# Kernel tuning notes

Measured on AMD Instinct MI355X. Metric: run time of the kernel, lower is better.

## Reference

```python
import jax, jax.numpy as jnp
import numpy as np

B, IN_DIM, CTRL, N_LOC, LOC_SZ, OUT = 2048, 512, 512, 65536, 64, 1
EPS = 1e-8


def setup_inputs() -> dict:
    key = jax.random.key(0)
    ks = jax.random.split(key, 11)
    s = 0.02
    return {
        "x": jax.random.normal(ks[0], (B, IN_DIM), dtype=jnp.float32),
        # Controller: h = tanh(x W_h + b_h), gate = x W_g + b_g
        "W_h": jax.random.normal(ks[1], (IN_DIM, CTRL), dtype=jnp.float32) * s,
        "b_h": jnp.zeros((CTRL,), dtype=jnp.float32),
        "W_g": jax.random.normal(ks[2], (IN_DIM, 1), dtype=jnp.float32) * s,
        "b_g": jnp.zeros((1,), dtype=jnp.float32),
        # Head read-key net: key = tanh(h W_k + b_k)
        "W_k": jax.random.normal(ks[3], (CTRL, LOC_SZ), dtype=jnp.float32) * s,
        "b_k": jnp.zeros((LOC_SZ,), dtype=jnp.float32),
        # Memory matrix [locations, location_size]
        "M": jax.random.normal(ks[4], (N_LOC, LOC_SZ), dtype=jnp.float32),
        # Output linear: (ctrl_dim + location_size) -> output_dim
        "W_out": jax.random.normal(ks[5], (CTRL + LOC_SZ, OUT), dtype=jnp.float32) * s,
        "b_out": jnp.zeros((OUT,), dtype=jnp.float32),
    }


def reference(x, W_h, b_h, W_g, b_g, W_k, b_k, M, W_out, b_out):
    # Vectorized version of the original per-sample Python loop.
    h = jnp.tanh(x @ W_h + b_h)                # [B, ctrl_dim]
    gate = x @ W_g + b_g                       # [B, 1]
    read_key = jnp.tanh(h @ W_k + b_k)         # [B, loc_sz]
    # Cosine-similarity content addressing over memory rows.
    kn = read_key / (jnp.linalg.norm(read_key, axis=-1, keepdims=True) + EPS)
    Mn = M / (jnp.linalg.norm(M, axis=-1, keepdims=True) + EPS)
    sim = kn @ Mn.T                            # [B, locations]
    w_read = jax.nn.softmax(sim, axis=-1)      # [B, locations]
    r = w_read @ M                             # [B, loc_sz]
    feat = jnp.concatenate([h, r], axis=-1)    # [B, ctrl_dim + loc_sz]
    output = (feat @ W_out + b_out)[:, 0]      # [B]
    # Original returns last-iteration h, gate, w_read alongside output.
    return output, h[-1], gate[-1], w_read[-1]
```

## Files before the change

### kernel.cpp

```cpp
#include <hip/hip_runtime.h>

#define B_SZ 2048
#define IN_DIM 512
#define CTRL 512
#define N_LOC 65536
#define NSPLIT 64
#define LPS (N_LOC / NSPLIT)
#define EPSV 1e-8f
#define LOG2E 1.4426950408889634f

typedef __attribute__((ext_vector_type(8))) short bf16x8;
typedef __attribute__((ext_vector_type(4))) float f32x4;
typedef __attribute__((ext_vector_type(16))) float f32x16;
typedef __attribute__((ext_vector_type(4))) unsigned int u32x4;
typedef __attribute__((ext_vector_type(8))) unsigned short u16x8;

static __device__ __forceinline__ unsigned int cvtpk(float lo, float hi) {
  unsigned int r;
  asm("v_cvt_pk_bf16_f32 %0, %1, %2" : "=v"(r) : "v"(lo), "v"(hi));
  return r;
}
static __device__ __forceinline__ unsigned short f2bf_hw(float f) {
  return (unsigned short)(cvtpk(f, f) & 0xffffu);
}
static __device__ __forceinline__ float bf2f(unsigned short u) {
  return __builtin_bit_cast(float, ((unsigned int)u) << 16);
}
static __device__ __forceinline__ float exp2_fast(float x) {
  float r;
  asm("v_exp_f32 %0, %1" : "=v"(r) : "v"(x));
  return r;
}

__global__ __launch_bounds__(256) void k_mega(const float* __restrict__ x,
                                              const float* __restrict__ Wh,
                                              const float* __restrict__ Wk,
                                              const float* __restrict__ M,
                                              const float* __restrict__ bh,
                                              unsigned short* __restrict__ Wkt,
                                              unsigned short* __restrict__ Mn_t,
                                              unsigned short* __restrict__ Mt_t,
                                              float* __restrict__ h) {
  const int bx = blockIdx.x, t = threadIdx.x;
  if (bx < 1024) {
    const int b = bx;
    const int c4 = t & 15, lg = t >> 4;
    float vv[4][4], ss[4];
#pragma unroll
    for (int r = 0; r < 4; r++) {
      const int loc = b * 64 + lg * 4 + r;
      const float4 f = *(const float4*)&M[(size_t)loc * 64 + c4 * 4];
      vv[r][0] = f.x; vv[r][1] = f.y; vv[r][2] = f.z; vv[r][3] = f.w;
      ss[r] = f.x * f.x + f.y * f.y + f.z * f.z + f.w * f.w;
    }
#pragma unroll
    for (int r = 0; r < 4; r++)
#pragma unroll
      for (int off = 1; off < 16; off <<= 1) ss[r] += __shfl_xor(ss[r], off);
#pragma unroll
    for (int r = 0; r < 4; r++) {
      const float s = (1.f / (sqrtf(ss[r]) + EPSV)) * LOG2E;
      uint2 u;
      u.x = cvtpk(vv[r][0] * s, vv[r][1] * s);
      u.y = cvtpk(vv[r][2] * s, vv[r][3] * s);
      *(uint2*)&Mn_t[(size_t)b * 4096 + (lg * 4 + r) * 64 + c4 * 4] = u;
    }
#pragma unroll
    for (int j = 0; j < 4; j++) {
      uint2 u;
      u.x = cvtpk(vv[0][j], vv[1][j]);
      u.y = cvtpk(vv[2][j], vv[3][j]);
      *(uint2*)&Mt_t[(size_t)b * 4096 + (c4 * 4 + j) * 64 + lg * 4] = u;
    }
  } else if (bx < 1032) {
    __shared__ float ld[64][65];
    const int ti = bx - 1024;
#pragma unroll
    for (int i = 0; i < 4; i++) {
      const int c = t + i * 256;
      const int r = c >> 4, cc4 = (c & 15) * 4;
      const float4 v = *(const float4*)&Wk[(size_t)(ti * 64 + r) * 64 + cc4];
      ld[r][cc4] = v.x; ld[r][cc4 + 1] = v.y; ld[r][cc4 + 2] = v.z; ld[r][cc4 + 3] = v.w;
    }
    __syncthreads();
#pragma unroll
    for (int i = 0; i < 2; i++) {
      const int c = t + i * 256;
      const int col = c >> 3, k8 = (c & 7) * 8;
      u16x8 o;
#pragma unroll
      for (int j = 0; j < 4; j++) {
        unsigned int u = cvtpk(ld[k8 + 2 * j][col], ld[k8 + 2 * j + 1][col]);
        o[2 * j] = (unsigned short)u;
        o[2 * j + 1] = (unsigned short)(u >> 16);
      }
      *(u16x8*)&Wkt[(size_t)col * IN_DIM + ti * 64 + k8] = o;
    }
  } else {
    __shared__ __align__(16) unsigned short xs[64 * 40];
    __shared__ __align__(16) unsigned short whs[64 * 40];
    const int id2 = bx - 1032;
    const int bm = (id2 & 31) * 64, bn = (id2 >> 5) * 64;
    const int lane = t & 63, wv = t >> 6, lo = lane & 15, g = lane >> 4;
    f32x4 acc[4];
#pragma unroll
    for (int ct = 0; ct < 4; ct++) acc[ct] = (f32x4){0.f, 0.f, 0.f, 0.f};
    for (int k0 = 0; k0 < IN_DIM; k0 += 32) {
#pragma unroll
      for (int i = 0; i < 2; i++) {
        const int lin = t + i * 256;
        const int r = lin >> 3, q = lin & 7;
        const float4 v = *(const float4*)&x[(size_t)(bm + r) * IN_DIM + k0 + q * 4];
        uint2 u;
        u.x = cvtpk(v.x, v.y);
        u.y = cvtpk(v.z, v.w);
        *(uint2*)&xs[r * 40 + q * 4] = u;
      }
#pragma unroll
      for (int i = 0; i < 2; i++) {
        const int lin = t + i * 256;
        const int kk = lin >> 4, q = lin & 15;
        const float4 v = *(const float4*)&Wh[(size_t)(k0 + kk) * CTRL + bn + q * 4];
        const unsigned int a = cvtpk(v.x, v.y), b2 = cvtpk(v.z, v.w);
        whs[(q * 4 + 0) * 40 + kk] = (unsigned short)a;
        whs[(q * 4 + 1) * 40 + kk] = (unsigned short)(a >> 16);
        whs[(q * 4 + 2) * 40 + kk] = (unsigned short)b2;
        whs[(q * 4 + 3) * 40 + kk] = (unsigned short)(b2 >> 16);
      }
      __syncthreads();
      const bf16x8 afr = *(const bf16x8*)&xs[(16 * wv + lo) * 40 + 8 * g];
#pragma unroll
      for (int ct = 0; ct < 4; ct++) {
        const bf16x8 bfr = *(const bf16x8*)&whs[(16 * ct + lo) * 40 + 8 * g];
        acc[ct] = __builtin_amdgcn_mfma_f32_16x16x32_bf16(afr, bfr, acc[ct], 0, 0, 0);
      }
      __syncthreads();
    }
#pragma unroll
    for (int ct = 0; ct < 4; ct++)
#pragma unroll
      for (int q = 0; q < 4; q++) {
        const int row = bm + 16 * wv + 4 * g + q;
        const int col = bn + 16 * ct + lo;
        h[(size_t)row * CTRL + col] = tanhf(acc[ct][q] + bh[col]);
      }
  }
}

__global__ __launch_bounds__(256) void k_readkey(const float* __restrict__ h_,
                                                 const unsigned short* __restrict__ Wkt,
                                                 const float* __restrict__ bk,
                                                 const float* __restrict__ x,
                                                 const float* __restrict__ Wg,
                                                 const float* __restrict__ bg,
                                                 unsigned short* __restrict__ kn_bf,
                                                 float* __restrict__ out) {
  __shared__ float sAcc[4][32][65];
  __shared__ float red[4];
  const int t = threadIdx.x, lane = t & 63, w = t >> 6;
  const int l31 = lane & 31, hh = lane >> 5;
  if (blockIdx.x < 64) {
    const int row0 = blockIdx.x * 32;
    f32x16 acc[2];
    acc[0] = (f32x16)(0.f); acc[1] = (f32x16)(0.f);
#pragma unroll
    for (int kk = 0; kk < 8; kk++) {
      const int kb = 128 * w + 16 * kk + 8 * hh;
      const float4 a0 = *(const float4*)&h_[(size_t)(row0 + l31) * CTRL + kb];
      const float4 a1 = *(const float4*)&h_[(size_t)(row0 + l31) * CTRL + kb + 4];
      const u32x4 av = {cvtpk(a0.x, a0.y), cvtpk(a0.z, a0.w), cvtpk(a1.x, a1.y), cvtpk(a1.z, a1.w)};
      const bf16x8 afr = __builtin_bit_cast(bf16x8, av);
#pragma unroll
      for (int ct = 0; ct < 2; ct++) {
        const bf16x8 bfr = *(const bf16x8*)&Wkt[(size_t)(32 * ct + l31) * IN_DIM + kb];
        acc[ct] = __builtin_amdgcn_mfma_f32_32x32x16_bf16(afr, bfr, acc[ct], 0, 0, 0);
      }
    }
#pragma unroll
    for (int ct = 0; ct < 2; ct++)
#pragma unroll
      for (int r = 0; r < 16; r++)
        sAcc[w][(r & 3) + 8 * (r >> 2) + 4 * hh][32 * ct + l31] = acc[ct][r];
    __syncthreads();
    const int row = t >> 3, c8 = (t & 7) * 8;
    float v[8];
    float ss = 0.f;
#pragma unroll
    for (int j = 0; j < 8; j++) {
      const float s = sAcc[0][row][c8 + j] + sAcc[1][row][c8 + j] +
                      sAcc[2][row][c8 + j] + sAcc[3][row][c8 + j] + bk[c8 + j];
      v[j] = tanhf(s);
      ss += v[j] * v[j];
    }
    ss += __shfl_xor(ss, 1);
    ss += __shfl_xor(ss, 2);
    ss += __shfl_xor(ss, 4);
    const float inv = 1.f / (sqrtf(ss) + EPSV);
    u16x8 o;
#pragma unroll
    for (int j = 0; j < 4; j++) {
      const unsigned int u = cvtpk(v[2 * j] * inv, v[2 * j + 1] * inv);
      o[2 * j] = (unsigned short)u;
      o[2 * j + 1] = (unsigned short)(u >> 16);
    }
    *(u16x8*)&kn_bf[(size_t)(row0 + row) * 64 + c8] = o;
  } else {
    out[2048 + t] = h_[(size_t)(B_SZ - 1) * CTRL + t];
    out[2048 + 256 + t] = h_[(size_t)(B_SZ - 1) * CTRL + 256 + t];
    float p = x[(size_t)(B_SZ - 1) * IN_DIM + t] * Wg[t] +
              x[(size_t)(B_SZ - 1) * IN_DIM + 256 + t] * Wg[256 + t];
#pragma unroll
    for (int off = 32; off >= 1; off >>= 1) p += __shfl_xor(p, off);
    if ((t & 63) == 0) red[t >> 6] = p;
    __syncthreads();
    if (t == 0) out[2048 + 512] = red[0] + red[1] + red[2] + red[3] + bg[0];
  }
}

__global__ __launch_bounds__(256, 2) void k_attn(const unsigned short* __restrict__ kn_bf,
                                                 const unsigned short* __restrict__ Mn_t,
                                                 const unsigned short* __restrict__ Mt_t,
                                                 float* __restrict__ l_part,
                                                 unsigned short* __restrict__ r_bf,
                                                 float* __restrict__ wdump) {
  __shared__ __align__(16) unsigned short sMn[2][4096];
  __shared__ __align__(16) unsigned short sMt[2][4096];
  const int sp = blockIdx.x, rb = blockIdx.y;
  const int t = threadIdx.x, lane = t & 63, w = t >> 6;
  const int l31 = lane & 31, hh = lane >> 5, l7 = lane & 7;
  const int row0 = rb * 256 + 64 * w;

  bf16x8 bq[2][4];
#pragma unroll
  for (int rs = 0; rs < 2; rs++)
#pragma unroll
    for (int kk = 0; kk < 4; kk++)
      bq[rs][kk] =
          *(const bf16x8*)&kn_bf[(size_t)(row0 + 32 * rs + l31) * 64 + 16 * kk + 8 * hh];

  const int c0 = t, c1 = t + 256;
  const int r0 = c0 >> 3, d0 = r0 * 64 + (((c0 & 7) * 8) ^ ((r0 & 7) * 8));
  const int r1 = c1 >> 3, d1 = r1 * 64 + (((c1 & 7) * 8) ^ ((r1 & 7) * 8));
  {
    const size_t gb = (size_t)(sp * 16) * 4096;
    *(u16x8*)&sMn[0][d0] = *(const u16x8*)&Mn_t[gb + c0 * 8];
    *(u16x8*)&sMn[0][d1] = *(const u16x8*)&Mn_t[gb + c1 * 8];
    *(u16x8*)&sMt[0][d0] = *(const u16x8*)&Mt_t[gb + c0 * 8];
    *(u16x8*)&sMt[0][d1] = *(const u16x8*)&Mt_t[gb + c1 * 8];
  }
  __syncthreads();

  f32x16 Racc[2][2];
#pragma unroll
  for (int rs = 0; rs < 2; rs++)
#pragma unroll
    for (int dt = 0; dt < 2; dt++) Racc[rs][dt] = (f32x16)(0.f);
  float lr0a = 0.f, lr0b = 0.f, lr1a = 0.f, lr1b = 0.f;

  u16x8 rn0, rn1, rt0, rt1;
  for (int it = 0; it < 16; ++it) {
    const int cur = it & 1;
    if (it < 15) {
      const size_t gn = (size_t)(sp * 16 + it + 1) * 4096;
      rn0 = *(const u16x8*)&Mn_t[gn + c0 * 8];
      rn1 = *(const u16x8*)&Mn_t[gn + c1 * 8];
      rt0 = *(const u16x8*)&Mt_t[gn + c0 * 8];
      rt1 = *(const u16x8*)&Mt_t[gn + c1 * 8];
    }

    f32x16 cst[2][2];
#pragma unroll
    for (int rs = 0; rs < 2; rs++)
#pragma unroll
      for (int lt = 0; lt < 2; lt++) cst[rs][lt] = (f32x16)(0.f);
    __builtin_amdgcn_s_setprio(1);
#pragma unroll
    for (int kk = 0; kk < 4; kk++) {
      const int koff = ((2 * kk + hh) ^ l7) * 8;
      const bf16x8 a0 = *(const bf16x8*)&sMn[cur][l31 * 64 + koff];
      const bf16x8 a1 = *(const bf16x8*)&sMn[cur][(32 + l31) * 64 + koff];
      cst[0][0] = __builtin_amdgcn_mfma_f32_32x32x16_bf16(a0, bq[0][kk], cst[0][0], 0, 0, 0);
      cst[0][1] = __builtin_amdgcn_mfma_f32_32x32x16_bf16(a1, bq[0][kk], cst[0][1], 0, 0, 0);
      cst[1][0] = __builtin_amdgcn_mfma_f32_32x32x16_bf16(a0, bq[1][kk], cst[1][0], 0, 0, 0);
      cst[1][1] = __builtin_amdgcn_mfma_f32_32x32x16_bf16(a1, bq[1][kk], cst[1][1], 0, 0, 0);
    }
    __builtin_amdgcn_s_setprio(0);

#pragma unroll
    for (int r = 0; r < 16; r++) {
      cst[0][0][r] = exp2_fast(cst[0][0][r]); lr0a += cst[0][0][r];
      cst[0][1][r] = exp2_fast(cst[0][1][r]); lr0b += cst[0][1][r];
      cst[1][0][r] = exp2_fast(cst[1][0][r]); lr1a += cst[1][0][r];
      cst[1][1][r] = exp2_fast(cst[1][1][r]); lr1b += cst[1][1][r];
    }

    if (rb == 7 && w == 3 && l31 == 31) {
#pragma unroll
      for (int lt = 0; lt < 2; lt++)
#pragma unroll
        for (int rr = 0; rr < 4; rr++)
          *(float4*)&wdump[sp * 1024 + it * 64 + 32 * lt + 8 * rr + 4 * hh] =
              make_float4(cst[1][lt][4 * rr], cst[1][lt][4 * rr + 1], cst[1][lt][4 * rr + 2],
                          cst[1][lt][4 * rr + 3]);
    }

    unsigned int pkq[2][2][8];
#pragma unroll
    for (int rs = 0; rs < 2; rs++)
#pragma unroll
      for (int lt = 0; lt < 2; lt++)
#pragma unroll
        for (int m = 0; m < 8; m++)
          pkq[rs][lt][m] = cvtpk(cst[rs][lt][2 * m], cst[rs][lt][2 * m + 1]);

#pragma unroll
    for (int kk = 0; kk < 4; kk++) {
      const int lt = kk >> 1, e4 = (kk & 1) * 4;
      const int koff = ((2 * kk + hh) ^ l7) * 8;
      const bf16x8 b0f = *(const bf16x8*)&sMt[cur][l31 * 64 + koff];
      const bf16x8 b1f = *(const bf16x8*)&sMt[cur][(32 + l31) * 64 + koff];
      __builtin_amdgcn_s_setprio(1);
#pragma unroll
      for (int rs = 0; rs < 2; rs++) {
        auto s0 = __builtin_amdgcn_permlane32_swap(pkq[rs][lt][e4 + 2], pkq[rs][lt][e4 + 0],
                                                   false, false);
        auto s1 = __builtin_amdgcn_permlane32_swap(pkq[rs][lt][e4 + 3], pkq[rs][lt][e4 + 1],
                                                   false, false);
        const u32x4 aw = {(unsigned int)s0[1], (unsigned int)s1[1], (unsigned int)s0[0],
                          (unsigned int)s1[0]};
        const bf16x8 afr = __builtin_bit_cast(bf16x8, aw);
        Racc[rs][0] = __builtin_amdgcn_mfma_f32_32x32x16_bf16(afr, b0f, Racc[rs][0], 0, 0, 0);
        Racc[rs][1] = __builtin_amdgcn_mfma_f32_32x32x16_bf16(afr, b1f, Racc[rs][1], 0, 0, 0);
      }
      __builtin_amdgcn_s_setprio(0);
    }

    if (it < 15) {
      const int nxt = cur ^ 1;
      *(u16x8*)&sMn[nxt][d0] = rn0; *(u16x8*)&sMn[nxt][d1] = rn1;
      *(u16x8*)&sMt[nxt][d0] = rt0; *(u16x8*)&sMt[nxt][d1] = rt1;
    }
    __syncthreads();
  }

  float lr0 = lr0a + lr0b, lr1 = lr1a + lr1b;
  lr0 += __shfl_xor(lr0, 32);
  lr1 += __shfl_xor(lr1, 32);
  if (hh == 0) {
    l_part[(size_t)(row0 + l31) * NSPLIT + sp] = lr0;
    l_part[(size_t)(row0 + 32 + l31) * NSPLIT + sp] = lr1;
  }

#pragma unroll
  for (int rs = 0; rs < 2; rs++)
#pragma unroll
    for (int dt = 0; dt < 2; dt++)
#pragma unroll
      for (int r = 0; r < 16; r++) {
        const int brow = (r & 3) + 8 * (r >> 2) + 4 * hh;
        r_bf[((size_t)(row0 + 32 * rs + brow) * NSPLIT + sp) * 64 + 32 * dt + l31] =
            f2bf_hw(Racc[rs][dt][r]);
      }
}

__global__ __launch_bounds__(256) void k_post(const float* __restrict__ l_part,
                                              const unsigned short* __restrict__ r_bf,
                                              const float* __restrict__ h,
                                              const float* __restrict__ Wout,
                                              const float* __restrict__ bout,
                                              const float* __restrict__ wdump,
                                              float* __restrict__ out) {
  const int lane = threadIdx.x & 63, w = threadIdx.x >> 6;
  const int bx = blockIdx.x;
  if (bx < 512) {
    const int row = bx * 4 + w;
    float l = l_part[(size_t)row * NSPLIT + lane];
#pragma unroll
    for (int off = 32; off >= 1; off >>= 1) l += __shfl_xor(l, off);
    float rd = 0.f;
    for (int sp2 = 0; sp2 < NSPLIT; sp2++)
      rd += bf2f(r_bf[((size_t)row * NSPLIT + sp2) * 64 + lane]);
    rd /= l;
    float acc = Wout[CTRL + lane] * rd;
    for (int k = lane; k < CTRL; k += 64) acc += h[(size_t)row * CTRL + k] * Wout[k];
#pragma unroll
    for (int off = 32; off >= 1; off >>= 1) acc += __shfl_xor(acc, off);
    if (lane == 0) out[row] = acc + bout[0];
  } else {
    float l = l_part[(size_t)(B_SZ - 1) * NSPLIT + lane];
#pragma unroll
    for (int off = 32; off >= 1; off >>= 1) l += __shfl_xor(l, off);
    const float rl = 1.f / l;
    const int i = ((bx - 512) * 256 + threadIdx.x) * 4;
    const float4 v = *(const float4*)&wdump[i];
    *(float4*)&out[2048 + 512 + 1 + i] = make_float4(v.x * rl, v.y * rl, v.z * rl, v.w * rl);
  }
}

extern "C" void kernel_launch(void* const* d_in, const int* in_sizes, int n_in,
                              void* d_out, int out_size, void* d_ws, size_t ws_size,
                              hipStream_t stream) {
  const float* x = (const float*)d_in[0];
  const float* Wh = (const float*)d_in[1];
  const float* bh = (const float*)d_in[2];
  const float* Wg = (const float*)d_in[3];
  const float* bg = (const float*)d_in[4];
  const float* Wk = (const float*)d_in[5];
  const float* bk = (const float*)d_in[6];
  const float* M = (const float*)d_in[7];
  const float* Wout = (const float*)d_in[8];
  const float* bout = (const float*)d_in[9];
  float* out = (float*)d_out;

  float* ws = (float*)d_ws;
  float* h = ws;
  float* l_part = h + 1048576;
  float* wdump = l_part + 131072;
  unsigned short* r_bf = (unsigned short*)(wdump + 65536);
  unsigned short* kn_bf = r_bf + 8388608;
  unsigned short* Mn_t = kn_bf + 131072;
  unsigned short* Mt_t = Mn_t + 4194304;
  unsigned short* Wkt = Mt_t + 4194304;

  hipLaunchKernelGGL(k_mega, dim3(1288), dim3(256), 0, stream,
                     x, Wh, Wk, M, bh, Wkt, Mn_t, Mt_t, h);
  hipLaunchKernelGGL(k_readkey, dim3(65), dim3(256), 0, stream,
                     h, Wkt, bk, x, Wg, bg, kn_bf, out);
  hipLaunchKernelGGL(k_attn, dim3(NSPLIT, 8), dim3(256), 0, stream,
                     kn_bf, Mn_t, Mt_t, l_part, r_bf, wdump);
  hipLaunchKernelGGL(k_post, dim3(512 + 64), dim3(256), 0, stream,
                     l_part, r_bf, h, Wout, bout, wdump, out);
}
```

Baseline: 80.63 us.

## Halve location splits and per-wave rows in attention, use nontemporal stores

The attention kernel now splits the 65536 memory locations into 32 chunks instead of 64, and each wave handles 32 query rows instead of 64. The grid becomes 32x16 blocks and each block loops over 32 location tiles. This halves the partial r and l buffers written to global memory and later reduced by k_post, but each wave does half the MFMA work per shared-memory tile, so the same Mn/Mt tiles are loaded by twice as many row blocks. Partial outputs also use nontemporal stores and loads to avoid polluting the cache.

```diff
diff --git a/kernel.cpp b/kernel.cpp
--- a/kernel.cpp
+++ b/kernel.cpp
@@ -4,7 +4,7 @@
 #define IN_DIM 512
 #define CTRL 512
 #define N_LOC 65536
-#define NSPLIT 64
+#define NSPLIT 32
 #define LPS (N_LOC / NSPLIT)
 #define EPSV 1e-8f
 #define LOG2E 1.4426950408889634f
@@ -228,21 +228,18 @@
   const int sp = blockIdx.x, rb = blockIdx.y;
   const int t = threadIdx.x, lane = t & 63, w = t >> 6;
   const int l31 = lane & 31, hh = lane >> 5, l7 = lane & 7;
-  const int row0 = rb * 256 + 64 * w;
-
-  bf16x8 bq[2][4];
-#pragma unroll
-  for (int rs = 0; rs < 2; rs++)
-#pragma unroll
-    for (int kk = 0; kk < 4; kk++)
-      bq[rs][kk] =
-          *(const bf16x8*)&kn_bf[(size_t)(row0 + 32 * rs + l31) * 64 + 16 * kk + 8 * hh];
+  const int row0 = rb * 128 + 32 * w;
+
+  bf16x8 bq[4];
+#pragma unroll
+  for (int kk = 0; kk < 4; kk++)
+    bq[kk] = *(const bf16x8*)&kn_bf[(size_t)(row0 + l31) * 64 + 16 * kk + 8 * hh];
 
   const int c0 = t, c1 = t + 256;
   const int r0 = c0 >> 3, d0 = r0 * 64 + (((c0 & 7) * 8) ^ ((r0 & 7) * 8));
   const int r1 = c1 >> 3, d1 = r1 * 64 + (((c1 & 7) * 8) ^ ((r1 & 7) * 8));
   {
-    const size_t gb = (size_t)(sp * 16) * 4096;
+    const size_t gb = (size_t)(sp * 32) * 4096;
     *(u16x8*)&sMn[0][d0] = *(const u16x8*)&Mn_t[gb + c0 * 8];
     *(u16x8*)&sMn[0][d1] = *(const u16x8*)&Mn_t[gb + c1 * 8];
     *(u16x8*)&sMt[0][d0] = *(const u16x8*)&Mt_t[gb + c0 * 8];
@@ -250,68 +247,61 @@
   }
   __syncthreads();
 
-  f32x16 Racc[2][2];
-#pragma unroll
-  for (int rs = 0; rs < 2; rs++)
-#pragma unroll
-    for (int dt = 0; dt < 2; dt++) Racc[rs][dt] = (f32x16)(0.f);
-  float lr0a = 0.f, lr0b = 0.f, lr1a = 0.f, lr1b = 0.f;
+  f32x16 Racc[2];
+  Racc[0] = (f32x16)(0.f); Racc[1] = (f32x16)(0.f);
+  float lra = 0.f, lrb = 0.f;
 
   u16x8 rn0, rn1, rt0, rt1;
-  for (int it = 0; it < 16; ++it) {
+  for (int it = 0; it < 32; ++it) {
     const int cur = it & 1;
-    if (it < 15) {
-      const size_t gn = (size_t)(sp * 16 + it + 1) * 4096;
+    if (it < 31) {
+      const size_t gn = (size_t)(sp * 32 + it + 1) * 4096;
       rn0 = *(const u16x8*)&Mn_t[gn + c0 * 8];
       rn1 = *(const u16x8*)&Mn_t[gn + c1 * 8];
       rt0 = *(const u16x8*)&Mt_t[gn + c0 * 8];
       rt1 = *(const u16x8*)&Mt_t[gn + c1 * 8];
     }
 
-    f32x16 cst[2][2];
-#pragma unroll
-    for (int rs = 0; rs < 2; rs++)
-#pragma unroll
-      for (int lt = 0; lt < 2; lt++) cst[rs][lt] = (f32x16)(0.f);
+    f32x16 cst[2];
+    cst[0] = (f32x16)(0.f); cst[1] = (f32x16)(0.f);
     __builtin_amdgcn_s_setprio(1);
 #pragma unroll
     for (int kk = 0; kk < 4; kk++) {
       const int koff = ((2 * kk + hh) ^ l7) * 8;
       const bf16x8 a0 = *(const bf16x8*)&sMn[cur][l31 * 64 + koff];
       const bf16x8 a1 = *(const bf16x8*)&sMn[cur][(32 + l31) * 64 + koff];
-      cst[0][0] = __builtin_amdgcn_mfma_f32_32x32x16_bf16(a0, bq[0][kk], cst[0][0], 0, 0, 0);
-      cst[0][1] = __builtin_amdgcn_mfma_f32_32x32x16_bf16(a1, bq[0][kk], cst[0][1], 0, 0, 0);
-      cst[1][0] = __builtin_amdgcn_mfma_f32_32x32x16_bf16(a0, bq[1][kk], cst[1][0], 0, 0, 0);
-      cst[1][1] = __builtin_amdgcn_mfma_f32_32x32x16_bf16(a1, bq[1][kk], cst[1][1], 0, 0, 0);
+      cst[0] = __builtin_amdgcn_mfma_f32_32x32x16_bf16(a0, bq[kk], cst[0], 0, 0, 0);
+      cst[1] = __builtin_amdgcn_mfma_f32_32x32x16_bf16(a1, bq[kk], cst[1], 0, 0, 0);
     }
     __builtin_amdgcn_s_setprio(0);
 
 #pragma unroll
     for (int r = 0; r < 16; r++) {
-      cst[0][0][r] = exp2_fast(cst[0][0][r]); lr0a += cst[0][0][r];
-      cst[0][1][r] = exp2_fast(cst[0][1][r]); lr0b += cst[0][1][r];
-      cst[1][0][r] = exp2_fast(cst[1][0][r]); lr1a += cst[1][0][r];
-      cst[1][1][r] = exp2_fast(cst[1][1][r]); lr1b += cst[1][1][r];
-    }
-
-    if (rb == 7 && w == 3 && l31 == 31) {
+      cst[0][r] = exp2_fast(cst[0][r]); lra += cst[0][r];
+      cst[1][r] = exp2_fast(cst[1][r]); lrb += cst[1][r];
+    }
+
+    if (rb == 15 && w == 3 && l31 == 31) {
 #pragma unroll
       for (int lt = 0; lt < 2; lt++)
 #pragma unroll
-        for (int rr = 0; rr < 4; rr++)
-          *(float4*)&wdump[sp * 1024 + it * 64 + 32 * lt + 8 * rr + 4 * hh] =
-              make_float4(cst[1][lt][4 * rr], cst[1][lt][4 * rr + 1], cst[1][lt][4 * rr + 2],
-                          cst[1][lt][4 * rr + 3]);
-    }
-
-    unsigned int pkq[2][2][8];
-#pragma unroll
-    for (int rs = 0; rs < 2; rs++)
-#pragma unroll
-      for (int lt = 0; lt < 2; lt++)
-#pragma unroll
-        for (int m = 0; m < 8; m++)
-          pkq[rs][lt][m] = cvtpk(cst[rs][lt][2 * m], cst[rs][lt][2 * m + 1]);
+        for (int rr = 0; rr < 4; rr++) {
+          const float4 o = make_float4(cst[lt][4 * rr], cst[lt][4 * rr + 1],
+                                       cst[lt][4 * rr + 2], cst[lt][4 * rr + 3]);
+          float* p = &wdump[sp * 2048 + it * 64 + 32 * lt + 8 * rr + 4 * hh];
+          __builtin_nontemporal_store(o.x, p + 0);
+          __builtin_nontemporal_store(o.y, p + 1);
+          __builtin_nontemporal_store(o.z, p + 2);
+          __builtin_nontemporal_store(o.w, p + 3);
+        }
+    }
+
+    unsigned int pkq[2][8];
+#pragma unroll
+    for (int lt = 0; lt < 2; lt++)
+#pragma unroll
+      for (int m = 0; m < 8; m++)
+        pkq[lt][m] = cvtpk(cst[lt][2 * m], cst[lt][2 * m + 1]);
 
 #pragma unroll
     for (int kk = 0; kk < 4; kk++) {
@@ -320,22 +310,19 @@
       const bf16x8 b0f = *(const bf16x8*)&sMt[cur][l31 * 64 + koff];
       const bf16x8 b1f = *(const bf16x8*)&sMt[cur][(32 + l31) * 64 + koff];
       __builtin_amdgcn_s_setprio(1);
-#pragma unroll
-      for (int rs = 0; rs < 2; rs++) {
-        auto s0 = __builtin_amdgcn_permlane32_swap(pkq[rs][lt][e4 + 2], pkq[rs][lt][e4 + 0],
-                                                   false, false);
-        auto s1 = __builtin_amdgcn_permlane32_swap(pkq[rs][lt][e4 + 3], pkq[rs][lt][e4 + 1],
-                                                   false, false);
-        const u32x4 aw = {(unsigned int)s0[1], (unsigned int)s1[1], (unsigned int)s0[0],
-                          (unsigned int)s1[0]};
-        const bf16x8 afr = __builtin_bit_cast(bf16x8, aw);
-        Racc[rs][0] = __builtin_amdgcn_mfma_f32_32x32x16_bf16(afr, b0f, Racc[rs][0], 0, 0, 0);
-        Racc[rs][1] = __builtin_amdgcn_mfma_f32_32x32x16_bf16(afr, b1f, Racc[rs][1], 0, 0, 0);
-      }
+      auto s0 = __builtin_amdgcn_permlane32_swap(pkq[lt][e4 + 2], pkq[lt][e4 + 0],
+                                                 false, false);
+      auto s1 = __builtin_amdgcn_permlane32_swap(pkq[lt][e4 + 3], pkq[lt][e4 + 1],
+                                                 false, false);
+      const u32x4 aw = {(unsigned int)s0[1], (unsigned int)s1[1], (unsigned int)s0[0],
+                        (unsigned int)s1[0]};
+      const bf16x8 afr = __builtin_bit_cast(bf16x8, aw);
+      Racc[0] = __builtin_amdgcn_mfma_f32_32x32x16_bf16(afr, b0f, Racc[0], 0, 0, 0);
+      Racc[1] = __builtin_amdgcn_mfma_f32_32x32x16_bf16(afr, b1f, Racc[1], 0, 0, 0);
       __builtin_amdgcn_s_setprio(0);
     }
 
-    if (it < 15) {
+    if (it < 31) {
       const int nxt = cur ^ 1;
       *(u16x8*)&sMn[nxt][d0] = rn0; *(u16x8*)&sMn[nxt][d1] = rn1;
       *(u16x8*)&sMt[nxt][d0] = rt0; *(u16x8*)&sMt[nxt][d1] = rt1;
@@ -343,24 +330,20 @@
     __syncthreads();
   }
 
-  float lr0 = lr0a + lr0b, lr1 = lr1a + lr1b;
-  lr0 += __shfl_xor(lr0, 32);
-  lr1 += __shfl_xor(lr1, 32);
-  if (hh == 0) {
-    l_part[(size_t)(row0 + l31) * NSPLIT + sp] = lr0;
-    l_part[(size_t)(row0 + 32 + l31) * NSPLIT + sp] = lr1;
-  }
-
-#pragma unroll
-  for (int rs = 0; rs < 2; rs++)
-#pragma unroll
-    for (int dt = 0; dt < 2; dt++)
-#pragma unroll
-      for (int r = 0; r < 16; r++) {
-        const int brow = (r & 3) + 8 * (r >> 2) + 4 * hh;
-        r_bf[((size_t)(row0 + 32 * rs + brow) * NSPLIT + sp) * 64 + 32 * dt + l31] =
-            f2bf_hw(Racc[rs][dt][r]);
-      }
+  float lr = lra + lrb;
+  lr += __shfl_xor(lr, 32);
+  if (hh == 0)
+    __builtin_nontemporal_store(lr, &l_part[(size_t)(row0 + l31) * NSPLIT + sp]);
+
+#pragma unroll
+  for (int dt = 0; dt < 2; dt++)
+#pragma unroll
+    for (int r = 0; r < 16; r++) {
+      const int brow = (r & 3) + 8 * (r >> 2) + 4 * hh;
+      __builtin_nontemporal_store(
+          f2bf_hw(Racc[dt][r]),
+          &r_bf[((size_t)(row0 + brow) * NSPLIT + sp) * 64 + 32 * dt + l31]);
+    }
 }
 
 __global__ __launch_bounds__(256) void k_post(const float* __restrict__ l_part,
@@ -374,12 +357,13 @@
   const int bx = blockIdx.x;
   if (bx < 512) {
     const int row = bx * 4 + w;
-    float l = l_part[(size_t)row * NSPLIT + lane];
+    float l = (lane < NSPLIT) ? l_part[(size_t)row * NSPLIT + lane] : 0.f;
 #pragma unroll
     for (int off = 32; off >= 1; off >>= 1) l += __shfl_xor(l, off);
     float rd = 0.f;
     for (int sp2 = 0; sp2 < NSPLIT; sp2++)
-      rd += bf2f(r_bf[((size_t)row * NSPLIT + sp2) * 64 + lane]);
+      rd += bf2f(__builtin_nontemporal_load(
+          &r_bf[((size_t)row * NSPLIT + sp2) * 64 + lane]));
     rd /= l;
     float acc = Wout[CTRL + lane] * rd;
     for (int k = lane; k < CTRL; k += 64) acc += h[(size_t)row * CTRL + k] * Wout[k];
@@ -387,7 +371,7 @@
     for (int off = 32; off >= 1; off >>= 1) acc += __shfl_xor(acc, off);
     if (lane == 0) out[row] = acc + bout[0];
   } else {
-    float l = l_part[(size_t)(B_SZ - 1) * NSPLIT + lane];
+    float l = (lane < NSPLIT) ? l_part[(size_t)(B_SZ - 1) * NSPLIT + lane] : 0.f;
 #pragma unroll
     for (int off = 32; off >= 1; off >>= 1) l += __shfl_xor(l, off);
     const float rl = 1.f / l;
@@ -415,9 +399,9 @@
   float* ws = (float*)d_ws;
   float* h = ws;
   float* l_part = h + 1048576;
-  float* wdump = l_part + 131072;
+  float* wdump = l_part + 65536;
   unsigned short* r_bf = (unsigned short*)(wdump + 65536);
-  unsigned short* kn_bf = r_bf + 8388608;
+  unsigned short* kn_bf = r_bf + 4194304;
   unsigned short* Mn_t = kn_bf + 131072;
   unsigned short* Mt_t = Mn_t + 4194304;
   unsigned short* Wkt = Mt_t + 4194304;
@@ -426,7 +410,7 @@
                      x, Wh, Wk, M, bh, Wkt, Mn_t, Mt_t, h);
   hipLaunchKernelGGL(k_readkey, dim3(65), dim3(256), 0, stream,
                      h, Wkt, bk, x, Wg, bg, kn_bf, out);
-  hipLaunchKernelGGL(k_attn, dim3(NSPLIT, 8), dim3(256), 0, stream,
+  hipLaunchKernelGGL(k_attn, dim3(NSPLIT, 16), dim3(256), 0, stream,
                      kn_bf, Mn_t, Mt_t, l_part, r_bf, wdump);
   hipLaunchKernelGGL(k_post, dim3(512 + 64), dim3(256), 0, stream,
                      l_part, r_bf, h, Wout, bout, wdump, out);
```

New measurement: 86.70 us. +7.5%, slower.
